# Kernel tuning notes

Measured on AMD Instinct MI355X. Metric: run time of the kernel, lower is better.

## Reference

```python
import jax, jax.numpy as jnp
import numpy as np

R = 16
N = 524288          # hash table size per level
F = 2               # features per entry
MIN_RES, MAX_RES = 16, 2048
PRIME = 2654435761  # spatial hash prime (as in the torch module)
H = R * F           # MLP width = 32
M = 1048576         # number of query points

# resolutions exactly as in NGP.__init__
RESOLUTIONS = np.round(
    np.logspace(np.log2(MIN_RES), np.log2(MAX_RES), R, base=2)
).astype(np.float32)


def setup_inputs() -> dict:
    key = jax.random.key(0)
    ks = jax.random.split(key, 8)
    coords = jax.random.uniform(ks[0], (M, 2), dtype=jnp.float32)
    hash_features = jax.random.normal(ks[1], (R, N, F), dtype=jnp.float32)
    s = 1.0 / np.sqrt(H)
    W0 = jax.random.uniform(ks[2], (H, H), dtype=jnp.float32, minval=-s, maxval=s)
    b0 = jax.random.uniform(ks[3], (H,), dtype=jnp.float32, minval=-s, maxval=s)
    W1 = jax.random.uniform(ks[4], (H, H), dtype=jnp.float32, minval=-s, maxval=s)
    b1 = jax.random.uniform(ks[5], (H,), dtype=jnp.float32, minval=-s, maxval=s)
    W2 = jax.random.uniform(ks[6], (H, 3), dtype=jnp.float32, minval=-s, maxval=s)
    b2 = jax.random.uniform(ks[7], (3,), dtype=jnp.float32, minval=-s, maxval=s)
    return {"coords": coords, "hash_features": hash_features,
            "W0": W0, "b0": b0, "W1": W1, "b1": b1, "W2": W2, "b2": b2}


def _bilerp_hash(coords, hash_features):
    """coords [M,2] in [0,1); hash_features [R,N,F] -> [M, R*F]."""
    res = jnp.asarray(RESOLUTIONS)  # [R]
    prime = jnp.uint32(PRIME)
    n = jnp.uint32(N)

    def level(res_r, table_r):  # table_r: [N,F]
        x = coords * res_r                    # [M,2]
        xf = jnp.floor(x)
        w = x - xf                            # bilinear weights [M,2]
        xi = xf.astype(jnp.uint32)
        x0, y0 = xi[:, 0], xi[:, 1]

        def look(xx, yy):
            idx = (xx ^ (prime * yy)) % n     # spatial hash
            return table_r[idx]               # gather [M,F]

        wx, wy = w[:, :1], w[:, 1:]
        return (look(x0, y0) * (1 - wx) * (1 - wy)
                + look(x0, y0 + 1) * (1 - wx) * wy
                + look(x0 + 1, y0) * wx * (1 - wy)
                + look(x0 + 1, y0 + 1) * wx * wy)  # [M,F]

    feats = jax.vmap(level)(res, hash_features)   # [R,M,F]
    return jnp.transpose(feats, (1, 0, 2)).reshape(coords.shape[0], -1)  # [M,R*F]


def reference(coords, hash_features, W0, b0, W1, b1, W2, b2):
    f = _bilerp_hash(coords, hash_features)          # [M, 32]
    h = jax.nn.leaky_relu(f @ W0 + b0, 0.01)
    h = jax.nn.leaky_relu(h @ W1 + b1, 0.01)
    return h @ W2 + b2                               # [M, 3]
```

## Files before the change

kernel.cpp:

```cpp
#include <hip/hip_runtime.h>
#include <cmath>

#define R_LEVELS 16
#define N_TAB    524288u
#define N_MASK   (N_TAB - 1u)
#define PRIME_H  2654435761u
#define M_PTS    1048576
#define BDIM     64
#define NBUCK    (BDIM * BDIM)
#define SBLK     64
#define STHR     1024
#define SPB      (M_PTS / SBLK)
#define SITER    (SPB / STHR)
#define XSTRIDE  36

typedef __attribute__((ext_vector_type(8)))  short bf16x8;
typedef __attribute__((ext_vector_type(16))) float f32x16;

union FragU { bf16x8 v; unsigned u[4]; uint2 u2[2]; };

struct ResArr { float r[R_LEVELS]; };

__device__ __forceinline__ unsigned pack_hi(float f0, float f1) {
    return __builtin_amdgcn_perm(__float_as_uint(f1), __float_as_uint(f0), 0x07060302u);
}
__device__ __forceinline__ unsigned pack_lo(float f0, float f1) {
    const float l0 = f0 - __uint_as_float(__float_as_uint(f0) & 0xffff0000u);
    const float l1 = f1 - __uint_as_float(__float_as_uint(f1) & 0xffff0000u);
    unsigned r;
    asm("v_cvt_pk_bf16_f32 %0, %1, %2" : "=v"(r) : "v"(l0), "v"(l1));
    return r;
}

__device__ __forceinline__ unsigned bucket_of(float x, float y) {
    unsigned bx = (unsigned)(x * (float)BDIM); if (bx >= BDIM) bx = BDIM - 1;
    unsigned by = (unsigned)(y * (float)BDIM); if (by >= BDIM) by = BDIM - 1;
    unsigned m = 0;
    #pragma unroll
    for (int i = 0; i < 6; ++i)
        m |= (((bx >> i) & 1u) << (2 * i)) | (((by >> i) & 1u) << (2 * i + 1));
    return m;
}

__global__ __launch_bounds__(STHR) void hist_k(const float2* __restrict__ coords,
                                               unsigned* __restrict__ C) {
    __shared__ unsigned h[NBUCK];
    const int t = threadIdx.x;
    const int w = blockIdx.x;
    #pragma unroll
    for (int i = t; i < NBUCK; i += STHR) h[i] = 0u;
    __syncthreads();
    #pragma unroll
    for (int k = 0; k < SITER; ++k) {
        const int p = w * SPB + k * STHR + t;
        const float2 c = coords[p];
        atomicAdd(&h[bucket_of(c.x, c.y)], 1u);
    }
    __syncthreads();
    #pragma unroll
    for (int i = t; i < NBUCK; i += STHR) C[(size_t)w * NBUCK + i] = h[i];
}

__global__ __launch_bounds__(256) void scanw_k(unsigned* __restrict__ C,
                                               unsigned* __restrict__ T) {
    const int b = blockIdx.x * 256 + threadIdx.x;
    unsigned s = 0;
    for (int w = 0; w < SBLK; ++w) {
        const size_t i = (size_t)w * NBUCK + b;
        const unsigned v = C[i];
        C[i] = s;
        s += v;
    }
    T[b] = s;
}

__global__ __launch_bounds__(256) void scan_k(const unsigned* __restrict__ T,
                                              unsigned* __restrict__ B) {
    __shared__ unsigned part[256];
    const int t = threadIdx.x;
    unsigned loc[16];
    unsigned sum = 0;
    #pragma unroll
    for (int k = 0; k < 16; ++k) {
        const unsigned c = T[t * 16 + k];
        loc[k] = sum;
        sum += c;
    }
    part[t] = sum;
    __syncthreads();
    for (int off = 1; off < 256; off <<= 1) {
        const unsigned v = (t >= off) ? part[t - off] : 0u;
        __syncthreads();
        part[t] += v;
        __syncthreads();
    }
    const unsigned base = (t > 0) ? part[t - 1] : 0u;
    #pragma unroll
    for (int k = 0; k < 16; ++k)
        B[t * 16 + k] = base + loc[k];
}

__global__ __launch_bounds__(STHR) void scatter_k(const float2* __restrict__ coords,
                                                  const unsigned* __restrict__ C,
                                                  const unsigned* __restrict__ B,
                                                  float2* __restrict__ sxy,
                                                  unsigned* __restrict__ sidx) {
    __shared__ unsigned off[NBUCK];
    const int t = threadIdx.x;
    const int w = blockIdx.x;
    #pragma unroll
    for (int i = t; i < NBUCK; i += STHR)
        off[i] = B[i] + C[(size_t)w * NBUCK + i];
    __syncthreads();
    #pragma unroll
    for (int k = 0; k < SITER; ++k) {
        const int p = w * SPB + k * STHR + t;
        const float2 c = coords[p];
        const unsigned b = bucket_of(c.x, c.y);
        const unsigned pos = atomicAdd(&off[b], 1u);
        sxy[pos] = c;
        sidx[pos] = (unsigned)p;
    }
}

__global__ __launch_bounds__(256) void ngp_mfma(
    const float2* __restrict__ pts,
    const unsigned* __restrict__ sidx,
    const float* __restrict__ hashf,
    const float* __restrict__ W0, const float* __restrict__ b0,
    const float* __restrict__ W1, const float* __restrict__ b1,
    const float* __restrict__ W2, const float* __restrict__ b2,
    float* __restrict__ out, ResArr res)
{
    __shared__ unsigned short Xh[256 * XSTRIDE];
    __shared__ unsigned short Xl[256 * XSTRIDE];

    const unsigned nwg = gridDim.x;
    const unsigned chunk = nwg >> 3;
    const unsigned sb = (blockIdx.x & 7u) * chunk + (blockIdx.x >> 3);
    const int tid = threadIdx.x;
    const int pb = (int)(sb * 256u);

    const float2 c = pts[pb + tid];

    float f[32];
    #pragma unroll
    for (int r = 0; r < R_LEVELS; ++r) {
        const float rr = res.r[r];
        const float x = c.x * rr;
        const float y = c.y * rr;
        const float xf = floorf(x);
        const float yf = floorf(y);
        const float wx = x - xf;
        const float wy = y - yf;
        const unsigned x0 = (unsigned)xf;
        const unsigned y0 = (unsigned)yf;
        const unsigned hy0 = PRIME_H * y0;
        const unsigned hy1 = PRIME_H * (y0 + 1u);
        const unsigned i00 = (x0 ^ hy0) & N_MASK;
        const unsigned i01 = (x0 ^ hy1) & N_MASK;
        const unsigned i10 = ((x0 + 1u) ^ hy0) & N_MASK;
        const unsigned i11 = ((x0 + 1u) ^ hy1) & N_MASK;
        const float2* tab = (const float2*)hashf + (size_t)r * N_TAB;
        const float2 v00 = tab[i00];
        const float2 v01 = tab[i01];
        const float2 v10 = tab[i10];
        const float2 v11 = tab[i11];
        const float w00 = (1.f - wx) * (1.f - wy);
        const float w01 = (1.f - wx) * wy;
        const float w10 = wx * (1.f - wy);
        const float w11 = wx * wy;
        f[2*r+0] = v00.x*w00 + v01.x*w01 + v10.x*w10 + v11.x*w11;
        f[2*r+1] = v00.y*w00 + v01.y*w01 + v10.y*w10 + v11.y*w11;
    }

    {
        const int rowo = tid * XSTRIDE;
        #pragma unroll
        for (int q = 0; q < 8; ++q) {
            uint2 ph, pl;
            ph.x = pack_hi(f[4*q+0], f[4*q+1]);
            ph.y = pack_hi(f[4*q+2], f[4*q+3]);
            pl.x = pack_lo(f[4*q+0], f[4*q+1]);
            pl.y = pack_lo(f[4*q+2], f[4*q+3]);
            *(uint2*)&Xh[rowo + 4*q] = ph;
            *(uint2*)&Xl[rowo + 4*q] = pl;
        }
    }

    const int lane = tid & 63;
    const int wv   = tid >> 6;
    const int l31  = lane & 31;
    const int h    = lane >> 5;
    const int tb0  = wv * 64;
    const int tb1  = wv * 64 + 32;

    auto ldx = [&](const unsigned short* X, int ptl, int kc) -> bf16x8 {
        FragU r;
        const int off = ptl * XSTRIDE + kc * 16 + h * 4;
        r.u2[0] = *(const uint2*)&X[off];
        r.u2[1] = *(const uint2*)&X[off + 8];
        return r.v;
    };

    auto wfrag = [&](const float* W, int ncol, int kc, bf16x8& fh, bf16x8& fl) {
        float wv8[8];
        #pragma unroll
        for (int e = 0; e < 8; ++e) {
            const int k = kc*16 + (e>>2)*8 + h*4 + (e&3);
            wv8[e] = (l31 < ncol) ? W[k*ncol + l31] : 0.f;
        }
        FragU H, L;
        #pragma unroll
        for (int w = 0; w < 4; ++w) {
            H.u[w] = pack_hi(wv8[2*w], wv8[2*w+1]);
            L.u[w] = pack_lo(wv8[2*w], wv8[2*w+1]);
        }
        fh = H.v; fl = L.v;
    };

    auto bias16 = [&](const float* b, int nvalid) -> f32x16 {
        f32x16 a;
        #pragma unroll
        for (int r = 0; r < 16; ++r) {
            const int rw = (r&3) + 8*(r>>2) + 4*h;
            a[r] = (rw < nvalid) ? b[rw] : 0.f;
        }
        return a;
    };

    auto layer = [&](const float* W, const float* b, int ncol, f32x16& a0, f32x16& a1) {
        a0 = bias16(b, ncol);
        a1 = bias16(b, ncol);
        #pragma unroll
        for (int kc = 0; kc < 2; ++kc) {
            bf16x8 wh, wl;
            wfrag(W, ncol, kc, wh, wl);
            {
                bf16x8 xh = ldx(Xh, tb0 + l31, kc);
                bf16x8 xl = ldx(Xl, tb0 + l31, kc);
                a0 = __builtin_amdgcn_mfma_f32_32x32x16_bf16(wh, xh, a0, 0, 0, 0);
                a0 = __builtin_amdgcn_mfma_f32_32x32x16_bf16(wh, xl, a0, 0, 0, 0);
                a0 = __builtin_amdgcn_mfma_f32_32x32x16_bf16(wl, xh, a0, 0, 0, 0);
            }
            {
                bf16x8 yh = ldx(Xh, tb1 + l31, kc);
                bf16x8 yl = ldx(Xl, tb1 + l31, kc);
                a1 = __builtin_amdgcn_mfma_f32_32x32x16_bf16(wh, yh, a1, 0, 0, 0);
                a1 = __builtin_amdgcn_mfma_f32_32x32x16_bf16(wh, yl, a1, 0, 0, 0);
                a1 = __builtin_amdgcn_mfma_f32_32x32x16_bf16(wl, yh, a1, 0, 0, 0);
            }
        }
    };

    auto store_act = [&](const f32x16& a, int ptl) {
        const int rowo = ptl * XSTRIDE;
        #pragma unroll
        for (int q = 0; q < 4; ++q) {
            float v0 = a[4*q+0], v1 = a[4*q+1], v2 = a[4*q+2], v3 = a[4*q+3];
            v0 = fmaxf(v0, 0.01f*v0);
            v1 = fmaxf(v1, 0.01f*v1);
            v2 = fmaxf(v2, 0.01f*v2);
            v3 = fmaxf(v3, 0.01f*v3);
            uint2 ph, pl;
            ph.x = pack_hi(v0, v1); ph.y = pack_hi(v2, v3);
            pl.x = pack_lo(v0, v1); pl.y = pack_lo(v2, v3);
            const int off = rowo + 8*q + 4*h;
            *(uint2*)&Xh[off] = ph;
            *(uint2*)&Xl[off] = pl;
        }
    };

    f32x16 a0, a1;
    layer(W0, b0, 32, a0, a1);
    store_act(a0, tb0 + l31);
    store_act(a1, tb1 + l31);
    layer(W1, b1, 32, a0, a1);
    store_act(a0, tb0 + l31);
    store_act(a1, tb1 + l31);
    layer(W2, b2, 3, a0, a1);

    if (h == 0) {
        const int pg0 = pb + tb0 + l31;
        const int pg1 = pb + tb1 + l31;
        const unsigned o0 = sidx ? sidx[pg0] : (unsigned)pg0;
        const unsigned o1 = sidx ? sidx[pg1] : (unsigned)pg1;
        out[(size_t)o0*3 + 0] = a0[0];
        out[(size_t)o0*3 + 1] = a0[1];
        out[(size_t)o0*3 + 2] = a0[2];
        out[(size_t)o1*3 + 0] = a1[0];
        out[(size_t)o1*3 + 1] = a1[1];
        out[(size_t)o1*3 + 2] = a1[2];
    }
}

extern "C" void kernel_launch(void* const* d_in, const int* in_sizes, int n_in,
                              void* d_out, int out_size, void* d_ws, size_t ws_size,
                              hipStream_t stream) {
    ResArr res;
    for (int i = 0; i < R_LEVELS; ++i)
        res.r[i] = (float)nearbyint(exp2(4.0 + (7.0 / 15.0) * (double)i));
    res.r[0] = 16.f;
    res.r[R_LEVELS - 1] = 2048.f;

    const float2* coords = (const float2*)d_in[0];
    const float* hashf   = (const float*)d_in[1];
    const float* W0      = (const float*)d_in[2];
    const float* b0      = (const float*)d_in[3];
    const float* W1      = (const float*)d_in[4];
    const float* b1      = (const float*)d_in[5];
    const float* W2      = (const float*)d_in[6];
    const float* b2      = (const float*)d_in[7];
    float* out           = (float*)d_out;

    const size_t off_C    = 0;
    const size_t off_T    = off_C + (size_t)SBLK * NBUCK * 4;
    const size_t off_B    = off_T + NBUCK * 4;
    const size_t off_sxy  = off_B + NBUCK * 4;
    const size_t off_sidx = off_sxy + (size_t)M_PTS * sizeof(float2);
    const size_t need     = off_sidx + (size_t)M_PTS * sizeof(unsigned);

    dim3 blockM(256);
    dim3 gridM(M_PTS / 256);

    if (ws_size >= need) {
        unsigned* C    = (unsigned*)((char*)d_ws + off_C);
        unsigned* T    = (unsigned*)((char*)d_ws + off_T);
        unsigned* B    = (unsigned*)((char*)d_ws + off_B);
        float2*   sxy  = (float2*)((char*)d_ws + off_sxy);
        unsigned* sidx = (unsigned*)((char*)d_ws + off_sidx);

        hipLaunchKernelGGL(hist_k,    dim3(SBLK), dim3(STHR), 0, stream, coords, C);
        hipLaunchKernelGGL(scanw_k,   dim3(NBUCK / 256), dim3(256), 0, stream, C, T);
        hipLaunchKernelGGL(scan_k,    dim3(1), dim3(256), 0, stream, T, B);
        hipLaunchKernelGGL(scatter_k, dim3(SBLK), dim3(STHR), 0, stream, coords, C, B, sxy, sidx);
        hipLaunchKernelGGL(ngp_mfma,  gridM, blockM, 0, stream,
                           sxy, sidx, hashf, W0, b0, W1, b1, W2, b2, out, res);
    } else {
        hipLaunchKernelGGL(ngp_mfma,  gridM, blockM, 0, stream,
                           coords, (const unsigned*)nullptr, hashf,
                           W0, b0, W1, b1, W2, b2, out, res);
    }
}
```

Measured before the change: 125.6 us.

## Prepack MLP weights, refine spatial sort buckets, drop sorted coord copy

The spatial sort grid goes from 64x64 to 128x128 Z-order buckets, with 16-bit per-block counts. The sorted coordinate copy is dropped, so the main kernel gathers coords through the sorted index. A new one-wave kernel packs the weights into bf16 hi/lo MFMA fragments once per call, so each wave no longer converts them itself. Hash gathers are grouped in batches of 8 levels to expose more memory-level parallelism. The costs are an extra launch, an indirect coordinate gather, and more registers held by the batched loads.

```diff
diff --git a/kernel.cpp b/kernel.cpp
--- a/kernel.cpp
+++ b/kernel.cpp
@@ -6,18 +6,19 @@
 #define N_MASK   (N_TAB - 1u)
 #define PRIME_H  2654435761u
 #define M_PTS    1048576
-#define BDIM     64
+#define BDIM     128
 #define NBUCK    (BDIM * BDIM)
 #define SBLK     64
 #define STHR     1024
 #define SPB      (M_PTS / SBLK)
 #define SITER    (SPB / STHR)
 #define XSTRIDE  36
+#define NFRAG    384
 
 typedef __attribute__((ext_vector_type(8)))  short bf16x8;
 typedef __attribute__((ext_vector_type(16))) float f32x16;
 
-union FragU { bf16x8 v; unsigned u[4]; uint2 u2[2]; };
+union FragU { bf16x8 v; uint4 q; unsigned u[4]; uint2 u2[2]; unsigned short s[8]; };
 
 struct ResArr { float r[R_LEVELS]; };
 
@@ -37,13 +38,13 @@
     unsigned by = (unsigned)(y * (float)BDIM); if (by >= BDIM) by = BDIM - 1;
     unsigned m = 0;
     #pragma unroll
-    for (int i = 0; i < 6; ++i)
+    for (int i = 0; i < 7; ++i)
         m |= (((bx >> i) & 1u) << (2 * i)) | (((by >> i) & 1u) << (2 * i + 1));
     return m;
 }
 
 __global__ __launch_bounds__(STHR) void hist_k(const float2* __restrict__ coords,
-                                               unsigned* __restrict__ C) {
+                                               unsigned short* __restrict__ C) {
     __shared__ unsigned h[NBUCK];
     const int t = threadIdx.x;
     const int w = blockIdx.x;
@@ -58,17 +59,18 @@
     }
     __syncthreads();
     #pragma unroll
-    for (int i = t; i < NBUCK; i += STHR) C[(size_t)w * NBUCK + i] = h[i];
-}
-
-__global__ __launch_bounds__(256) void scanw_k(unsigned* __restrict__ C,
+    for (int i = t; i < NBUCK; i += STHR)
+        C[(size_t)w * NBUCK + i] = (unsigned short)h[i];
+}
+
+__global__ __launch_bounds__(256) void scanw_k(unsigned short* __restrict__ C,
                                                unsigned* __restrict__ T) {
     const int b = blockIdx.x * 256 + threadIdx.x;
     unsigned s = 0;
     for (int w = 0; w < SBLK; ++w) {
         const size_t i = (size_t)w * NBUCK + b;
         const unsigned v = C[i];
-        C[i] = s;
+        C[i] = (unsigned short)s;
         s += v;
     }
     T[b] = s;
@@ -78,14 +80,8 @@
                                               unsigned* __restrict__ B) {
     __shared__ unsigned part[256];
     const int t = threadIdx.x;
-    unsigned loc[16];
     unsigned sum = 0;
-    #pragma unroll
-    for (int k = 0; k < 16; ++k) {
-        const unsigned c = T[t * 16 + k];
-        loc[k] = sum;
-        sum += c;
-    }
+    for (int k = 0; k < 64; ++k) sum += T[t * 64 + k];
     part[t] = sum;
     __syncthreads();
     for (int off = 1; off < 256; off <<= 1) {
@@ -94,23 +90,23 @@
         part[t] += v;
         __syncthreads();
     }
-    const unsigned base = (t > 0) ? part[t - 1] : 0u;
-    #pragma unroll
-    for (int k = 0; k < 16; ++k)
-        B[t * 16 + k] = base + loc[k];
+    unsigned run = (t > 0) ? part[t - 1] : 0u;
+    for (int k = 0; k < 64; ++k) {
+        B[t * 64 + k] = run;
+        run += T[t * 64 + k];
+    }
 }
 
 __global__ __launch_bounds__(STHR) void scatter_k(const float2* __restrict__ coords,
-                                                  const unsigned* __restrict__ C,
+                                                  const unsigned short* __restrict__ C,
                                                   const unsigned* __restrict__ B,
-                                                  float2* __restrict__ sxy,
                                                   unsigned* __restrict__ sidx) {
     __shared__ unsigned off[NBUCK];
     const int t = threadIdx.x;
     const int w = blockIdx.x;
     #pragma unroll
     for (int i = t; i < NBUCK; i += STHR)
-        off[i] = B[i] + C[(size_t)w * NBUCK + i];
+        off[i] = B[i] + (unsigned)C[(size_t)w * NBUCK + i];
     __syncthreads();
     #pragma unroll
     for (int k = 0; k < SITER; ++k) {
@@ -118,18 +114,50 @@
         const float2 c = coords[p];
         const unsigned b = bucket_of(c.x, c.y);
         const unsigned pos = atomicAdd(&off[b], 1u);
-        sxy[pos] = c;
         sidx[pos] = (unsigned)p;
     }
 }
 
+__global__ __launch_bounds__(64) void wprep_k(const float* __restrict__ W0,
+                                              const float* __restrict__ W1,
+                                              const float* __restrict__ W2,
+                                              const float* __restrict__ b2,
+                                              uint4* __restrict__ wbuf,
+                                              float* __restrict__ b2p) {
+    const int lane = threadIdx.x;
+    const int l31 = lane & 31;
+    const int h   = lane >> 5;
+    const float* Ws[3] = {W0, W1, W2};
+    const int ncols[3] = {32, 32, 3};
+    for (int l = 0; l < 3; ++l) {
+        for (int kc = 0; kc < 2; ++kc) {
+            FragU H, L;
+            for (int e = 0; e < 8; ++e) {
+                const int k = kc*16 + (e>>2)*8 + h*4 + (e&3);
+                const float w = (l31 < ncols[l]) ? Ws[l][k*ncols[l] + l31] : 0.f;
+                const unsigned short hi = (unsigned short)(__float_as_uint(w) >> 16);
+                const float rem = w - __uint_as_float((unsigned)hi << 16);
+                const unsigned u = __float_as_uint(rem);
+                const unsigned short lo = (unsigned short)((u + 0x7fffu + ((u >> 16) & 1u)) >> 16);
+                H.s[e] = hi;
+                L.s[e] = lo;
+            }
+            const int fi = (l*2 + kc)*64 + lane;
+            wbuf[fi]         = H.q;
+            wbuf[NFRAG + fi] = L.q;
+        }
+    }
+    if (lane < 32) b2p[lane] = (lane < 3) ? b2[lane] : 0.f;
+}
+
 __global__ __launch_bounds__(256) void ngp_mfma(
-    const float2* __restrict__ pts,
+    const float2* __restrict__ coords,
     const unsigned* __restrict__ sidx,
     const float* __restrict__ hashf,
-    const float* __restrict__ W0, const float* __restrict__ b0,
-    const float* __restrict__ W1, const float* __restrict__ b1,
-    const float* __restrict__ W2, const float* __restrict__ b2,
+    const uint4* __restrict__ wbuf,
+    const float* __restrict__ b0,
+    const float* __restrict__ b1,
+    const float* __restrict__ b2p,
     float* __restrict__ out, ResArr res)
 {
     __shared__ unsigned short Xh[256 * XSTRIDE];
@@ -139,39 +167,51 @@
     const unsigned chunk = nwg >> 3;
     const unsigned sb = (blockIdx.x & 7u) * chunk + (blockIdx.x >> 3);
     const int tid = threadIdx.x;
-    const int pb = (int)(sb * 256u);
-
-    const float2 c = pts[pb + tid];
+    const int p = (int)(sb * 256u) + tid;
+
+    const unsigned oid = sidx ? sidx[p] : (unsigned)p;
+    const float2 c = coords[oid];
 
     float f[32];
     #pragma unroll
-    for (int r = 0; r < R_LEVELS; ++r) {
-        const float rr = res.r[r];
-        const float x = c.x * rr;
-        const float y = c.y * rr;
-        const float xf = floorf(x);
-        const float yf = floorf(y);
-        const float wx = x - xf;
-        const float wy = y - yf;
-        const unsigned x0 = (unsigned)xf;
-        const unsigned y0 = (unsigned)yf;
-        const unsigned hy0 = PRIME_H * y0;
-        const unsigned hy1 = PRIME_H * (y0 + 1u);
-        const unsigned i00 = (x0 ^ hy0) & N_MASK;
-        const unsigned i01 = (x0 ^ hy1) & N_MASK;
-        const unsigned i10 = ((x0 + 1u) ^ hy0) & N_MASK;
-        const unsigned i11 = ((x0 + 1u) ^ hy1) & N_MASK;
-        const float2* tab = (const float2*)hashf + (size_t)r * N_TAB;
-        const float2 v00 = tab[i00];
-        const float2 v01 = tab[i01];
-        const float2 v10 = tab[i10];
-        const float2 v11 = tab[i11];
-        const float w00 = (1.f - wx) * (1.f - wy);
-        const float w01 = (1.f - wx) * wy;
-        const float w10 = wx * (1.f - wy);
-        const float w11 = wx * wy;
-        f[2*r+0] = v00.x*w00 + v01.x*w01 + v10.x*w10 + v11.x*w11;
-        f[2*r+1] = v00.y*w00 + v01.y*w01 + v10.y*w10 + v11.y*w11;
+    for (int ck = 0; ck < 2; ++ck) {
+        float2 v00[8], v01[8], v10[8], v11[8];
+        float wxs[8], wys[8];
+        #pragma unroll
+        for (int j = 0; j < 8; ++j) {
+            const int r = ck * 8 + j;
+            const float rr = res.r[r];
+            const float x = c.x * rr;
+            const float y = c.y * rr;
+            const float xf = floorf(x);
+            const float yf = floorf(y);
+            wxs[j] = x - xf;
+            wys[j] = y - yf;
+            const unsigned x0 = (unsigned)xf;
+            const unsigned y0 = (unsigned)yf;
+            const unsigned hy0 = PRIME_H * y0;
+            const unsigned hy1 = PRIME_H * (y0 + 1u);
+            const unsigned i00 = (x0 ^ hy0) & N_MASK;
+            const unsigned i01 = (x0 ^ hy1) & N_MASK;
+            const unsigned i10 = ((x0 + 1u) ^ hy0) & N_MASK;
+            const unsigned i11 = ((x0 + 1u) ^ hy1) & N_MASK;
+            const float2* tab = (const float2*)hashf + (size_t)r * N_TAB;
+            v00[j] = tab[i00];
+            v01[j] = tab[i01];
+            v10[j] = tab[i10];
+            v11[j] = tab[i11];
+        }
+        #pragma unroll
+        for (int j = 0; j < 8; ++j) {
+            const float wx = wxs[j], wy = wys[j];
+            const float w00 = (1.f - wx) * (1.f - wy);
+            const float w01 = (1.f - wx) * wy;
+            const float w10 = wx * (1.f - wy);
+            const float w11 = wx * wy;
+            const int r = ck * 8 + j;
+            f[2*r+0] = v00[j].x*w00 + v01[j].x*w01 + v10[j].x*w10 + v11[j].x*w11;
+            f[2*r+1] = v00[j].y*w00 + v01[j].y*w01 + v10[j].y*w10 + v11[j].y*w11;
+        }
     }
 
     {
@@ -203,54 +243,53 @@
         return r.v;
     };
 
-    auto wfrag = [&](const float* W, int ncol, int kc, bf16x8& fh, bf16x8& fl) {
-        float wv8[8];
-        #pragma unroll
-        for (int e = 0; e < 8; ++e) {
-            const int k = kc*16 + (e>>2)*8 + h*4 + (e&3);
-            wv8[e] = (l31 < ncol) ? W[k*ncol + l31] : 0.f;
-        }
-        FragU H, L;
-        #pragma unroll
-        for (int w = 0; w < 4; ++w) {
-            H.u[w] = pack_hi(wv8[2*w], wv8[2*w+1]);
-            L.u[w] = pack_lo(wv8[2*w], wv8[2*w+1]);
-        }
-        fh = H.v; fl = L.v;
-    };
-
-    auto bias16 = [&](const float* b, int nvalid) -> f32x16 {
+    auto bias_init = [&](const float* b) -> f32x16 {
         f32x16 a;
         #pragma unroll
-        for (int r = 0; r < 16; ++r) {
-            const int rw = (r&3) + 8*(r>>2) + 4*h;
-            a[r] = (rw < nvalid) ? b[rw] : 0.f;
+        for (int q = 0; q < 4; ++q) {
+            const float4 t = *(const float4*)(b + 8*q + 4*h);
+            a[4*q+0] = t.x; a[4*q+1] = t.y; a[4*q+2] = t.z; a[4*q+3] = t.w;
         }
         return a;
     };
 
-    auto layer = [&](const float* W, const float* b, int ncol, f32x16& a0, f32x16& a1) {
-        a0 = bias16(b, ncol);
-        a1 = bias16(b, ncol);
-        #pragma unroll
-        for (int kc = 0; kc < 2; ++kc) {
-            bf16x8 wh, wl;
-            wfrag(W, ncol, kc, wh, wl);
-            {
-                bf16x8 xh = ldx(Xh, tb0 + l31, kc);
-                bf16x8 xl = ldx(Xl, tb0 + l31, kc);
-                a0 = __builtin_amdgcn_mfma_f32_32x32x16_bf16(wh, xh, a0, 0, 0, 0);
-                a0 = __builtin_amdgcn_mfma_f32_32x32x16_bf16(wh, xl, a0, 0, 0, 0);
-                a0 = __builtin_amdgcn_mfma_f32_32x32x16_bf16(wl, xh, a0, 0, 0, 0);
-            }
-            {
-                bf16x8 yh = ldx(Xh, tb1 + l31, kc);
-                bf16x8 yl = ldx(Xl, tb1 + l31, kc);
-                a1 = __builtin_amdgcn_mfma_f32_32x32x16_bf16(wh, yh, a1, 0, 0, 0);
-                a1 = __builtin_amdgcn_mfma_f32_32x32x16_bf16(wh, yl, a1, 0, 0, 0);
-                a1 = __builtin_amdgcn_mfma_f32_32x32x16_bf16(wl, yh, a1, 0, 0, 0);
-            }
-        }
+    auto layer = [&](int l, const float* b, f32x16& a0, f32x16& a1) {
+        FragU wh0, wl0, wh1, wl1;
+        wh0.q = wbuf[(l*2+0)*64 + lane];
+        wl0.q = wbuf[NFRAG + (l*2+0)*64 + lane];
+        wh1.q = wbuf[(l*2+1)*64 + lane];
+        wl1.q = wbuf[NFRAG + (l*2+1)*64 + lane];
+        f32x16 A0 = bias_init(b);
+        f32x16 A1 = A0;
+        {
+            const bf16x8 xh = ldx(Xh, tb0 + l31, 0);
+            const bf16x8 xl = ldx(Xl, tb0 + l31, 0);
+            A0 = __builtin_amdgcn_mfma_f32_32x32x16_bf16(wh0.v, xh, A0, 0, 0, 0);
+            A0 = __builtin_amdgcn_mfma_f32_32x32x16_bf16(wh0.v, xl, A0, 0, 0, 0);
+            A0 = __builtin_amdgcn_mfma_f32_32x32x16_bf16(wl0.v, xh, A0, 0, 0, 0);
+        }
+        {
+            const bf16x8 xh = ldx(Xh, tb1 + l31, 0);
+            const bf16x8 xl = ldx(Xl, tb1 + l31, 0);
+            A1 = __builtin_amdgcn_mfma_f32_32x32x16_bf16(wh0.v, xh, A1, 0, 0, 0);
+            A1 = __builtin_amdgcn_mfma_f32_32x32x16_bf16(wh0.v, xl, A1, 0, 0, 0);
+            A1 = __builtin_amdgcn_mfma_f32_32x32x16_bf16(wl0.v, xh, A1, 0, 0, 0);
+        }
+        {
+            const bf16x8 xh = ldx(Xh, tb0 + l31, 1);
+            const bf16x8 xl = ldx(Xl, tb0 + l31, 1);
+            A0 = __builtin_amdgcn_mfma_f32_32x32x16_bf16(wh1.v, xh, A0, 0, 0, 0);
+            A0 = __builtin_amdgcn_mfma_f32_32x32x16_bf16(wh1.v, xl, A0, 0, 0, 0);
+            A0 = __builtin_amdgcn_mfma_f32_32x32x16_bf16(wl1.v, xh, A0, 0, 0, 0);
+        }
+        {
+            const bf16x8 xh = ldx(Xh, tb1 + l31, 1);
+            const bf16x8 xl = ldx(Xl, tb1 + l31, 1);
+            A1 = __builtin_amdgcn_mfma_f32_32x32x16_bf16(wh1.v, xh, A1, 0, 0, 0);
+            A1 = __builtin_amdgcn_mfma_f32_32x32x16_bf16(wh1.v, xl, A1, 0, 0, 0);
+            A1 = __builtin_amdgcn_mfma_f32_32x32x16_bf16(wl1.v, xh, A1, 0, 0, 0);
+        }
+        a0 = A0; a1 = A1;
     };
 
     auto store_act = [&](const f32x16& a, int ptl) {
@@ -272,19 +311,19 @@
     };
 
     f32x16 a0, a1;
-    layer(W0, b0, 32, a0, a1);
+    layer(0, b0, a0, a1);
     store_act(a0, tb0 + l31);
     store_act(a1, tb1 + l31);
-    layer(W1, b1, 32, a0, a1);
+    layer(1, b1, a0, a1);
     store_act(a0, tb0 + l31);
     store_act(a1, tb1 + l31);
-    layer(W2, b2, 3, a0, a1);
+    layer(2, b2p, a0, a1);
 
     if (h == 0) {
-        const int pg0 = pb + tb0 + l31;
-        const int pg1 = pb + tb1 + l31;
-        const unsigned o0 = sidx ? sidx[pg0] : (unsigned)pg0;
-        const unsigned o1 = sidx ? sidx[pg1] : (unsigned)pg1;
+        const int pl0 = (int)(sb * 256u) + tb0 + l31;
+        const int pl1 = (int)(sb * 256u) + tb1 + l31;
+        const unsigned o0 = sidx ? sidx[pl0] : (unsigned)pl0;
+        const unsigned o1 = sidx ? sidx[pl1] : (unsigned)pl1;
         out[(size_t)o0*3 + 0] = a0[0];
         out[(size_t)o0*3 + 1] = a0[1];
         out[(size_t)o0*3 + 2] = a0[2];
@@ -314,31 +353,37 @@
     float* out           = (float*)d_out;
 
     const size_t off_C    = 0;
-    const size_t off_T    = off_C + (size_t)SBLK * NBUCK * 4;
+    const size_t off_T    = off_C + (size_t)SBLK * NBUCK * 2;
     const size_t off_B    = off_T + NBUCK * 4;
-    const size_t off_sxy  = off_B + NBUCK * 4;
-    const size_t off_sidx = off_sxy + (size_t)M_PTS * sizeof(float2);
-    const size_t need     = off_sidx + (size_t)M_PTS * sizeof(unsigned);
+    const size_t off_sidx = off_B + NBUCK * 4;
+    const size_t off_wbuf = off_sidx + (size_t)M_PTS * 4;
+    const size_t off_b2p  = off_wbuf + 2 * NFRAG * sizeof(uint4);
+    const size_t need     = off_b2p + 32 * sizeof(float);
+    const size_t need_min = 2 * NFRAG * sizeof(uint4) + 32 * sizeof(float);
 
     dim3 blockM(256);
     dim3 gridM(M_PTS / 256);
 
     if (ws_size >= need) {
-        unsigned* C    = (unsigned*)((char*)d_ws + off_C);
+        unsigned short* C = (unsigned short*)((char*)d_ws + off_C);
         unsigned* T    = (unsigned*)((char*)d_ws + off_T);
         unsigned* B    = (unsigned*)((char*)d_ws + off_B);
-        float2*   sxy  = (float2*)((char*)d_ws + off_sxy);
         unsigned* sidx = (unsigned*)((char*)d_ws + off_sidx);
-
+        uint4*    wbuf = (uint4*)((char*)d_ws + off_wbuf);
+        float*    b2p  = (float*)((char*)d_ws + off_b2p);
+
+        hipLaunchKernelGGL(wprep_k,   dim3(1), dim3(64), 0, stream, W0, W1, W2, b2, wbuf, b2p);
         hipLaunchKernelGGL(hist_k,    dim3(SBLK), dim3(STHR), 0, stream, coords, C);
         hipLaunchKernelGGL(scanw_k,   dim3(NBUCK / 256), dim3(256), 0, stream, C, T);
         hipLaunchKernelGGL(scan_k,    dim3(1), dim3(256), 0, stream, T, B);
-        hipLaunchKernelGGL(scatter_k, dim3(SBLK), dim3(STHR), 0, stream, coords, C, B, sxy, sidx);
+        hipLaunchKernelGGL(scatter_k, dim3(SBLK), dim3(STHR), 0, stream, coords, C, B, sidx);
         hipLaunchKernelGGL(ngp_mfma,  gridM, blockM, 0, stream,
-                           sxy, sidx, hashf, W0, b0, W1, b1, W2, b2, out, res);
-    } else {
+                           coords, sidx, hashf, wbuf, b0, b1, b2p, out, res);
+    } else if (ws_size >= need_min) {
+        uint4* wbuf = (uint4*)d_ws;
+        float* b2p  = (float*)((char*)d_ws + 2 * NFRAG * sizeof(uint4));
+        hipLaunchKernelGGL(wprep_k,   dim3(1), dim3(64), 0, stream, W0, W1, W2, b2, wbuf, b2p);
         hipLaunchKernelGGL(ngp_mfma,  gridM, blockM, 0, stream,
-                           coords, (const unsigned*)nullptr, hashf,
-                           W0, b0, W1, b1, W2, b2, out, res);
-    }
-}
+                           coords, (const unsigned*)nullptr, hashf, wbuf, b0, b1, b2p, out, res);
+    }
+}
```

Result: no change. 123.3 us (-1.8%).
